# Optimization experiments

Hardware: AMD Instinct MI355X
Metric: run time of the kernel (lower is better)

The kernel has to match this reference:

```python
import jax, jax.numpy as jnp
import numpy as np

NUM_GRAPHS = 512

def setup_inputs() -> dict:
    key = jax.random.key(0)
    ks = jax.random.split(key, 8)
    N, E, SD = 50000, 800000, 128
    x_ids = jax.random.randint(ks[0], (N,), 0, 1340)
    edge_index = jax.random.randint(ks[1], (2, E), 0, N)
    batch = jnp.sort(jax.random.randint(ks[2], (N,), 0, NUM_GRAPHS))
    emb = jax.random.normal(ks[3], (1340, SD), dtype=jnp.float32) * 0.1
    W1 = jax.random.normal(ks[4], (SD, 2 * SD), dtype=jnp.float32) * 0.1
    b1 = jnp.zeros((2 * SD,), dtype=jnp.float32)
    W2 = jax.random.normal(ks[5], (2 * SD, 41), dtype=jnp.float32) * 0.1
    b2 = jnp.zeros((41,), dtype=jnp.float32)
    return {"x_ids": x_ids, "edge_index": edge_index, "batch": batch,
            "emb": emb, "W1": W1, "b1": b1, "W2": W2, "b2": b2}

def _gcn_conv(x, src, dst, W, b, num_nodes):
    # x: [N, Fin] -> [N, Fout]; GCN: add self-loops, deg^-1/2 norm, transform, aggregate
    deg = jax.ops.segment_sum(jnp.ones_like(dst, dtype=x.dtype), dst, num_segments=num_nodes)
    dinv = jnp.where(deg > 0, jax.lax.rsqrt(jnp.where(deg > 0, deg, 1.0)), 0.0)
    norm = dinv[src] * dinv[dst]               # [E+N]
    h = x @ W                                  # [N, Fout]
    msg = h[src] * norm[:, None]               # [E+N, Fout] gather (memory-bound)
    out = jax.ops.segment_sum(msg, dst, num_segments=num_nodes)
    return out + b

def reference(x_ids, edge_index, batch, emb, W1, b1, W2, b2):
    N = x_ids.shape[0]
    loops = jnp.arange(N, dtype=edge_index.dtype)
    src = jnp.concatenate([edge_index[0], loops])
    dst = jnp.concatenate([edge_index[1], loops])
    x = emb[x_ids]                                   # embedding lookup [N, SD]
    x = _gcn_conv(x, src, dst, W1, b1, N)
    x = jax.nn.relu(x)                               # dropout is identity in eval mode
    x = _gcn_conv(x, src, dst, W2, b2, N)
    return jax.ops.segment_sum(x, batch, num_segments=NUM_GRAPHS)  # [512, 41]
```

## Files before the change

kernel.cpp:

```cpp
#include <hip/hip_runtime.h>

#define N_NODES 50000
#define N_EDGES 800000
#define N_TOT   850000
#define SD 128
#define HD 256
#define OD 41
#define ODP 48
#define NG 512
#define NB 128
#define NPB 391
#define BCAP 8192

typedef __attribute__((ext_vector_type(8))) short bh8;
typedef __attribute__((ext_vector_type(4))) float f4;
typedef unsigned long long u64;

__device__ inline unsigned short f2bf(float x) {
  unsigned u = __float_as_uint(x);
  unsigned r = u + 0x7fff + ((u >> 16) & 1);
  return (unsigned short)(r >> 16);
}
__device__ inline float bf2f(unsigned short s) {
  return __uint_as_float(((unsigned)s) << 16);
}
__device__ inline float bflo(unsigned e) { return __uint_as_float(e << 16); }
__device__ inline float bfhi(unsigned e) { return __uint_as_float(e & 0xffff0000u); }

__device__ inline unsigned rec_xid(u64 r)  { return ((unsigned)r) >> 16; }
__device__ inline unsigned rec_src(u64 r)  { return ((unsigned)r) & 0xFFFFu; }
__device__ inline float    rec_nrm(u64 r)  { return __uint_as_float((unsigned)(r >> 32) & 0xFFFF0000u); }

__global__ __launch_bounds__(256) void zero2_kernel(float4* __restrict__ a, int na,
                                                    float4* __restrict__ b, int nb) {
  int i = blockIdx.x * 256 + threadIdx.x;
  float4 z = make_float4(0.f, 0.f, 0.f, 0.f);
  if (i < na) { a[i] = z; return; }
  int j = i - na;
  if (j < nb) b[j] = z;
}

__global__ __launch_bounds__(256) void cvt_all_kernel(const float* __restrict__ emb,
    const float* __restrict__ W1, const float* __restrict__ W2,
    unsigned short* __restrict__ embb, unsigned short* __restrict__ w1f,
    unsigned short* __restrict__ w2f) {
  int tid = blockIdx.x * 256 + threadIdx.x;
  if (tid < 1340 * SD) { embb[tid] = f2bf(emb[tid]); return; }
  int u = tid - 1340 * SD;
  if (u < 4096) {
    int lane = u & 63, frag = u >> 6;
    int ks = frag >> 4, cf = frag & 15;
    int col = cf * 16 + (lane & 15);
    #pragma unroll
    for (int j = 0; j < 8; ++j) {
      int k = ks * 32 + ((lane >> 4) << 3) + j;
      w1f[u * 8 + j] = f2bf(W1[k * HD + col]);
    }
    return;
  }
  u -= 4096;
  if (u < 1536) {
    int lane = u & 63, frag = u >> 6;
    int ks = frag / 3, cf = frag % 3;
    int col = cf * 16 + (lane & 15);
    #pragma unroll
    for (int j = 0; j < 8; ++j) {
      int k = ks * 32 + ((lane >> 4) << 3) + j;
      w2f[u * 8 + j] = (col < OD) ? f2bf(W2[k * OD + col]) : (unsigned short)0;
    }
  }
}

__global__ __launch_bounds__(256) void passA_kernel(const int* __restrict__ ei,
    const int* __restrict__ x_ids, int* __restrict__ curB, u64* __restrict__ stage) {
  __shared__ int lcur[NB];
  __shared__ int base[NB];
  int t = threadIdx.x;
  if (t < NB) lcur[t] = 0;
  __syncthreads();
  u64 pay[16];
  int loc[16];
  int e0 = blockIdx.x * 4096;
  #pragma unroll
  for (int j = 0; j < 16; ++j) {
    int e = e0 + j * 256 + t;
    loc[j] = -1;
    if (e < N_TOT) {
      int s, d;
      if (e < N_EDGES) { s = ei[e]; d = ei[N_EDGES + e]; }
      else             { s = d = e - N_EDGES; }
      int b = d / NPB;
      int lofs = atomicAdd(&lcur[b], 1);
      loc[j] = (b << 13) | lofs;
      pay[j] = ((u64)(unsigned)x_ids[s] << 32) | ((u64)(unsigned)d << 16) | (u64)(unsigned)s;
    }
  }
  __syncthreads();
  if (t < NB) base[t] = atomicAdd(&curB[t], lcur[t]);
  __syncthreads();
  #pragma unroll
  for (int j = 0; j < 16; ++j) {
    if (loc[j] >= 0) {
      int b = loc[j] >> 13, lofs = loc[j] & 8191;
      stage[(size_t)b * BCAP + base[b] + lofs] = pay[j];
    }
  }
}

__global__ __launch_bounds__(256) void count_kernel(const int* __restrict__ curB,
    const u64* __restrict__ stage, int* __restrict__ vcnt, float* __restrict__ dinv) {
  __shared__ int cl[NPB];
  int t = threadIdx.x, k = blockIdx.x;
  for (int l = t; l < NPB; l += 256) cl[l] = 0;
  __syncthreads();
  int nbk = curB[k];
  const u64* st = stage + (size_t)k * BCAP;
  for (int i = t; i < nbk; i += 256) {
    int d = (int)((st[i] >> 16) & 0xFFFFu);
    atomicAdd(&cl[d - k * NPB], 1);
  }
  __syncthreads();
  int n0 = k * NPB;
  int nn = (n0 + NPB <= N_NODES) ? NPB : (N_NODES - n0);
  for (int l = t; l < nn; l += 256) {
    int v = cl[l];
    vcnt[n0 + l] = v;
    dinv[n0 + l] = rsqrtf((float)v);
  }
}

__global__ __launch_bounds__(256) void scan1_kernel(const int* __restrict__ vcnt,
    int* __restrict__ off, int* __restrict__ bsum) {
  __shared__ int lds[256];
  int t = threadIdx.x;
  int i = blockIdx.x * 256 + t;
  int v = (i < N_NODES) ? vcnt[i] : 0;
  lds[t] = v;
  __syncthreads();
  for (int s = 1; s < 256; s <<= 1) {
    int add = (t >= s) ? lds[t - s] : 0;
    __syncthreads();
    lds[t] += add;
    __syncthreads();
  }
  int inc = lds[t];
  if (i < N_NODES) off[i] = inc - v;
  if (t == 255) bsum[blockIdx.x] = inc;
}

__global__ __launch_bounds__(256) void scan2_kernel(int* __restrict__ bsum, int* __restrict__ bso, int nb) {
  __shared__ int lds[256];
  int t = threadIdx.x;
  int v = (t < nb) ? bsum[t] : 0;
  lds[t] = v;
  __syncthreads();
  for (int s = 1; s < 256; s <<= 1) {
    int add = (t >= s) ? lds[t - s] : 0;
    __syncthreads();
    lds[t] += add;
    __syncthreads();
  }
  if (t < nb) bso[t] = lds[t] - v;
}

__global__ __launch_bounds__(256) void scan3g_kernel(int* __restrict__ off,
    const int* __restrict__ bso, const int* __restrict__ batch, int* __restrict__ gstart) {
  int i = blockIdx.x * 256 + threadIdx.x;
  if (i < N_NODES) off[i] += bso[blockIdx.x];
  if (i == 0) off[N_NODES] = N_TOT;
  if (i < N_NODES) {
    if (i == 0) {
      for (int g = 0; g <= batch[0]; ++g) gstart[g] = 0;
    } else {
      int bp = batch[i - 1], bn = batch[i];
      for (int g = bp + 1; g <= bn; ++g) gstart[g] = i;
    }
    if (i == N_NODES - 1) {
      for (int g = batch[i] + 1; g <= NG; ++g) gstart[g] = N_NODES;
    }
  }
}

__global__ __launch_bounds__(256) void passB_kernel(const int* __restrict__ curB,
    const u64* __restrict__ stage, const int* __restrict__ off,
    const float* __restrict__ dinv, u64* __restrict__ rec) {
  __shared__ int lcur[NPB];
  __shared__ int loff[NPB];
  int t = threadIdx.x, k = blockIdx.x;
  int n0 = k * NPB;
  int nn = (n0 + NPB <= N_NODES) ? NPB : (N_NODES - n0);
  for (int l = t; l < nn; l += 256) { lcur[l] = 0; loff[l] = off[n0 + l]; }
  __syncthreads();
  int nbk = curB[k];
  const u64* st = stage + (size_t)k * BCAP;
  for (int i = t; i < nbk; i += 256) {
    u64 r = st[i];
    int s   = (int)(r & 0xFFFFu);
    int d   = (int)((r >> 16) & 0xFFFFu);
    int xid = (int)((r >> 32) & 0xFFFFu);
    float nrm = dinv[s] * dinv[d];
    int ld = d - n0;
    int p = loff[ld] + atomicAdd(&lcur[ld], 1);
    rec[p] = ((u64)f2bf(nrm) << 48) | ((u64)(unsigned)xid << 16) | (u64)(unsigned)s;
  }
}

__global__ __launch_bounds__(256) void agg1w_kernel(const int* __restrict__ off,
    const u64* __restrict__ rec, const unsigned int* __restrict__ embw,
    unsigned int* __restrict__ agg1w) {
  int lane = threadIdx.x & 63;
  int node = __builtin_amdgcn_readfirstlane(blockIdx.x * 4 + (threadIdx.x >> 6));
  int beg = off[node], end = off[node + 1];
  float a0 = 0.f, a1 = 0.f;
  int i = beg;
  for (; i + 8 <= end; i += 8) {
    u64 r[8];
    unsigned e[8];
    #pragma unroll
    for (int p = 0; p < 8; ++p) r[p] = rec[i + p];
    #pragma unroll
    for (int p = 0; p < 8; ++p) e[p] = embw[rec_xid(r[p]) * 64 + lane];
    #pragma unroll
    for (int p = 0; p < 8; ++p) {
      float n = rec_nrm(r[p]);
      a0 += n * bflo(e[p]); a1 += n * bfhi(e[p]);
    }
  }
  for (; i + 4 <= end; i += 4) {
    u64 r0 = rec[i], r1 = rec[i + 1], r2 = rec[i + 2], r3 = rec[i + 3];
    unsigned e0 = embw[rec_xid(r0) * 64 + lane];
    unsigned e1 = embw[rec_xid(r1) * 64 + lane];
    unsigned e2 = embw[rec_xid(r2) * 64 + lane];
    unsigned e3 = embw[rec_xid(r3) * 64 + lane];
    float n0 = rec_nrm(r0), n1 = rec_nrm(r1), n2 = rec_nrm(r2), n3 = rec_nrm(r3);
    a0 += n0 * bflo(e0); a1 += n0 * bfhi(e0);
    a0 += n1 * bflo(e1); a1 += n1 * bfhi(e1);
    a0 += n2 * bflo(e2); a1 += n2 * bfhi(e2);
    a0 += n3 * bflo(e3); a1 += n3 * bfhi(e3);
  }
  for (; i < end; ++i) {
    u64 r = rec[i];
    unsigned e = embw[rec_xid(r) * 64 + lane];
    float n = rec_nrm(r);
    a0 += n * bflo(e); a1 += n * bfhi(e);
  }
  unsigned packed = (unsigned)f2bf(a0) | ((unsigned)f2bf(a1) << 16);
  agg1w[node * 64 + lane] = packed;
}

__global__ __launch_bounds__(256) void gemm12_mfma(const unsigned short* __restrict__ agg1,
    const bh8* __restrict__ w1f, const float* __restrict__ b1,
    const bh8* __restrict__ w2f, unsigned short* __restrict__ h2b) {
  __shared__ char raw[32768];
  int t = threadIdx.x, lane = t & 63, wave = t >> 6;
  int row0 = blockIdx.x * 64;
  #pragma unroll
  for (int k = 0; k < 4; ++k) {
    int idx = k * 256 + t;
    int r = idx >> 4, cc = idx & 15;
    int4 v = make_int4(0, 0, 0, 0);
    if (row0 + r < N_NODES)
      v = *(const int4*)((const char*)agg1 + (size_t)(row0 + r) * 256 + cc * 16);
    *(int4*)(raw + ((r * 256 + cc * 16) ^ ((r & 15) << 4))) = v;
  }
  bh8 bf1[4][4];
  #pragma unroll
  for (int cf = 0; cf < 4; ++cf)
    #pragma unroll
    for (int ks = 0; ks < 4; ++ks)
      bf1[cf][ks] = w1f[(ks * 16 + wave * 4 + cf) * 64 + lane];
  f4 acc[4][4];
  #pragma unroll
  for (int rf = 0; rf < 4; ++rf)
    #pragma unroll
    for (int cf = 0; cf < 4; ++cf)
      acc[rf][cf] = (f4){0.f, 0.f, 0.f, 0.f};
  __syncthreads();
  #pragma unroll
  for (int ks = 0; ks < 4; ++ks) {
    bh8 a[4];
    #pragma unroll
    for (int rf = 0; rf < 4; ++rf) {
      int r = rf * 16 + (lane & 15);
      int byte = (r * 256 + ks * 64 + ((lane >> 4) << 4)) ^ ((r & 15) << 4);
      a[rf] = *(const bh8*)(raw + byte);
    }
    #pragma unroll
    for (int rf = 0; rf < 4; ++rf)
      #pragma unroll
      for (int cf = 0; cf < 4; ++cf)
        acc[rf][cf] = __builtin_amdgcn_mfma_f32_16x16x32_bf16(a[rf], bf1[cf][ks], acc[rf][cf], 0, 0, 0);
  }
  __syncthreads();
  #pragma unroll
  for (int cf = 0; cf < 4; ++cf) {
    int col = wave * 64 + cf * 16 + (lane & 15);
    float bias = b1[col];
    #pragma unroll
    for (int rf = 0; rf < 4; ++rf)
      #pragma unroll
      for (int j = 0; j < 4; ++j) {
        int r = rf * 16 + ((lane >> 4) << 2) + j;
        unsigned short v = f2bf(fmaxf(acc[rf][cf][j] + bias, 0.f));
        *(unsigned short*)(raw + ((r * 512 + col * 2) ^ ((r & 15) << 4))) = v;
      }
  }
  bh8 bf2[3][8];
  #pragma unroll
  for (int cf = 0; cf < 3; ++cf)
    #pragma unroll
    for (int ks = 0; ks < 8; ++ks)
      bf2[cf][ks] = w2f[(ks * 3 + cf) * 64 + lane];
  f4 acc2[3];
  #pragma unroll
  for (int cf = 0; cf < 3; ++cf) acc2[cf] = (f4){0.f, 0.f, 0.f, 0.f};
  __syncthreads();
  int r2 = wave * 16 + (lane & 15);
  #pragma unroll
  for (int ks = 0; ks < 8; ++ks) {
    int byte = (r2 * 512 + ks * 64 + ((lane >> 4) << 4)) ^ ((r2 & 15) << 4);
    bh8 a = *(const bh8*)(raw + byte);
    #pragma unroll
    for (int cf = 0; cf < 3; ++cf)
      acc2[cf] = __builtin_amdgcn_mfma_f32_16x16x32_bf16(a, bf2[cf][ks], acc2[cf], 0, 0, 0);
  }
  #pragma unroll
  for (int cf = 0; cf < 3; ++cf) {
    int col = cf * 16 + (lane & 15);
    #pragma unroll
    for (int j = 0; j < 4; ++j) {
      int rg = row0 + wave * 16 + ((lane >> 4) << 2) + j;
      if (rg < N_NODES)
        h2b[(size_t)rg * ODP + col] = f2bf(acc2[cf][j]);
    }
  }
}

__global__ __launch_bounds__(256) void pool2_kernel(const int* __restrict__ gstart,
    const int* __restrict__ off, const u64* __restrict__ rec,
    const unsigned short* __restrict__ h2b, const float* __restrict__ b2,
    float* __restrict__ out) {
  __shared__ float red[4][2][24][2];
  int g = blockIdx.x >> 3, c = blockIdx.x & 7;
  int t = threadIdx.x, lane = t & 63, wv = t >> 6;
  int n0 = gstart[g], n1 = gstart[g + 1];
  int e0 = off[n0], e1 = off[n1];
  int len = e1 - e0;
  int c0 = e0 + ((len * c) >> 3);
  int c1 = e0 + ((len * (c + 1)) >> 3);
  int clen = c1 - c0;
  int w0 = c0 + ((clen * wv) >> 2);
  int w1 = c0 + ((clen * (wv + 1)) >> 2);
  int half = (lane >= 24 && lane < 48) ? 1 : 0;
  int l24 = (lane < 24) ? lane : ((lane < 48) ? lane - 24 : lane - 48);
  float a0 = 0.f, a1 = 0.f;
  int i = w0;
  for (; i + 16 <= w1; i += 16) {
    u64 ra[8], rb[8];
    #pragma unroll
    for (int p = 0; p < 8; ++p) { ra[p] = rec[i + 2 * p]; rb[p] = rec[i + 2 * p + 1]; }
    #pragma unroll
    for (int p = 0; p < 8; ++p) {
      u64 r = half ? rb[p] : ra[p];
      unsigned hw = *(const unsigned*)(h2b + (size_t)rec_src(r) * ODP + l24 * 2);
      float n = rec_nrm(r);
      a0 += n * bflo(hw); a1 += n * bfhi(hw);
    }
  }
  for (; i < w1; ++i) {
    u64 r = rec[i];
    unsigned hw = *(const unsigned*)(h2b + (size_t)rec_src(r) * ODP + l24 * 2);
    float n = rec_nrm(r);
    if (lane < 24) { a0 += n * bflo(hw); a1 += n * bfhi(hw); }
  }
  if (lane < 48) { red[wv][half][l24][0] = a0; red[wv][half][l24][1] = a1; }
  __syncthreads();
  if (t < 48) {
    int m = t >> 1, b = t & 1;
    float s = red[0][0][m][b] + red[0][1][m][b] + red[1][0][m][b] + red[1][1][m][b]
            + red[2][0][m][b] + red[2][1][m][b] + red[3][0][m][b] + red[3][1][m][b];
    if (t < OD) {
      if (c == 0) s += (float)(n1 - n0) * b2[t];
      unsafeAtomicAdd(&out[g * OD + t], s);
    }
  }
}

extern "C" void kernel_launch(void* const* d_in, const int* in_sizes, int n_in,
                              void* d_out, int out_size, void* d_ws, size_t ws_size,
                              hipStream_t stream) {
  const int*   x_ids = (const int*)d_in[0];
  const int*   ei    = (const int*)d_in[1];
  const int*   batch = (const int*)d_in[2];
  const float* emb   = (const float*)d_in[3];
  const float* W1    = (const float*)d_in[4];
  const float* b1    = (const float*)d_in[5];
  const float* W2    = (const float*)d_in[6];
  const float* b2    = (const float*)d_in[7];
  float* out = (float*)d_out;
  char* ws = (char*)d_ws;

  int*            vcnt   = (int*)           (ws + 0);
  int*            curB   = (int*)           (ws + 204800);
  float*          dinv   = (float*)         (ws + 208896);
  int*            off    = (int*)           (ws + 413696);
  int*            bsum   = (int*)           (ws + 618496);
  int*            bso    = (int*)           (ws + 619520);
  int*            gstart = (int*)           (ws + 620544);
  unsigned short* embb   = (unsigned short*)(ws + 1048576);
  unsigned short* w1f    = (unsigned short*)(ws + 1441792);
  unsigned short* w2f    = (unsigned short*)(ws + 1507328);
  u64*            rec    = (u64*)           (ws + 2097152);
  u64*            stage  = (u64*)           (ws + 9437184);
  unsigned short* agg1   = (unsigned short*)(ws + 18874368);
  unsigned short* h2b    = (unsigned short*)(ws + 33554432);

  zero2_kernel<<<21, 256, 0, stream>>>((float4*)curB, 32, (float4*)out, 5248);
  cvt_all_kernel<<<692, 256, 0, stream>>>(emb, W1, W2, embb, w1f, w2f);

  passA_kernel<<<208, 256, 0, stream>>>(ei, x_ids, curB, stage);
  count_kernel<<<NB,  256, 0, stream>>>(curB, stage, vcnt, dinv);
  scan1_kernel<<<196, 256, 0, stream>>>(vcnt, off, bsum);
  scan2_kernel<<<1,   256, 0, stream>>>(bsum, bso, 196);
  scan3g_kernel<<<196, 256, 0, stream>>>(off, bso, batch, gstart);
  passB_kernel<<<NB,  256, 0, stream>>>(curB, stage, off, dinv, rec);

  agg1w_kernel<<<12500, 256, 0, stream>>>(off, rec, (const unsigned int*)embb, (unsigned int*)agg1);
  gemm12_mfma <<<782,   256, 0, stream>>>(agg1, (const bh8*)w1f, b1, (const bh8*)w2f, h2b);
  pool2_kernel<<<4096,  256, 0, stream>>>(gstart, off, rec, h2b, b2, out);
}
```

Before: 118.2 us.

## Widen gather loads to 16 bytes and fold small setup kernels together

The layer-1 aggregation now has each lane gather a 16-byte chunk of an embedding row, with four edges handled per wave at once, and reduces the partial sums across lanes with shuffles. The pooling pass likewise loads 16-byte chunks of h2 rows, ten edges per wave across 60 lanes, and reduces through a larger shared array. The zeroing kernel is merged into the conversion kernel, and the single-block scan2 is folded into scan3g, where every block redoes the 196-entry scan itself. Together these aim to cut memory instructions and launch count, at the cost of extra shuffle and reduction work and some idle lanes.

```diff
diff --git a/kernel.cpp b/kernel.cpp
--- a/kernel.cpp
+++ b/kernel.cpp
@@ -26,24 +26,18 @@
 }
 __device__ inline float bflo(unsigned e) { return __uint_as_float(e << 16); }
 __device__ inline float bfhi(unsigned e) { return __uint_as_float(e & 0xffff0000u); }
+__device__ inline unsigned pk2(float lo, float hi) {
+  return (unsigned)f2bf(lo) | ((unsigned)f2bf(hi) << 16);
+}
 
 __device__ inline unsigned rec_xid(u64 r)  { return ((unsigned)r) >> 16; }
 __device__ inline unsigned rec_src(u64 r)  { return ((unsigned)r) & 0xFFFFu; }
 __device__ inline float    rec_nrm(u64 r)  { return __uint_as_float((unsigned)(r >> 32) & 0xFFFF0000u); }
 
-__global__ __launch_bounds__(256) void zero2_kernel(float4* __restrict__ a, int na,
-                                                    float4* __restrict__ b, int nb) {
-  int i = blockIdx.x * 256 + threadIdx.x;
-  float4 z = make_float4(0.f, 0.f, 0.f, 0.f);
-  if (i < na) { a[i] = z; return; }
-  int j = i - na;
-  if (j < nb) b[j] = z;
-}
-
-__global__ __launch_bounds__(256) void cvt_all_kernel(const float* __restrict__ emb,
+__global__ __launch_bounds__(256) void init_kernel(const float* __restrict__ emb,
     const float* __restrict__ W1, const float* __restrict__ W2,
     unsigned short* __restrict__ embb, unsigned short* __restrict__ w1f,
-    unsigned short* __restrict__ w2f) {
+    unsigned short* __restrict__ w2f, float4* __restrict__ curB4, float4* __restrict__ out4) {
   int tid = blockIdx.x * 256 + threadIdx.x;
   if (tid < 1340 * SD) { embb[tid] = f2bf(emb[tid]); return; }
   int u = tid - 1340 * SD;
@@ -68,7 +62,13 @@
       int k = ks * 32 + ((lane >> 4) << 3) + j;
       w2f[u * 8 + j] = (col < OD) ? f2bf(W2[k * OD + col]) : (unsigned short)0;
     }
-  }
+    return;
+  }
+  u -= 1536;
+  float4 z = make_float4(0.f, 0.f, 0.f, 0.f);
+  if (u < 32) { curB4[u] = z; return; }
+  u -= 32;
+  if (u < 5248) out4[u] = z;
 }
 
 __global__ __launch_bounds__(256) void passA_kernel(const int* __restrict__ ei,
@@ -148,10 +148,11 @@
   if (t == 255) bsum[blockIdx.x] = inc;
 }
 
-__global__ __launch_bounds__(256) void scan2_kernel(int* __restrict__ bsum, int* __restrict__ bso, int nb) {
+__global__ __launch_bounds__(256) void scan3g_kernel(int* __restrict__ off,
+    const int* __restrict__ bsum, const int* __restrict__ batch, int* __restrict__ gstart) {
   __shared__ int lds[256];
   int t = threadIdx.x;
-  int v = (t < nb) ? bsum[t] : 0;
+  int v = (t < 196) ? bsum[t] : 0;
   lds[t] = v;
   __syncthreads();
   for (int s = 1; s < 256; s <<= 1) {
@@ -160,13 +161,10 @@
     lds[t] += add;
     __syncthreads();
   }
-  if (t < nb) bso[t] = lds[t] - v;
-}
-
-__global__ __launch_bounds__(256) void scan3g_kernel(int* __restrict__ off,
-    const int* __restrict__ bso, const int* __restrict__ batch, int* __restrict__ gstart) {
-  int i = blockIdx.x * 256 + threadIdx.x;
-  if (i < N_NODES) off[i] += bso[blockIdx.x];
+  int b = blockIdx.x;
+  int bso = (b == 0) ? 0 : lds[b - 1];
+  int i = b * 256 + t;
+  if (i < N_NODES) off[i] += bso;
   if (i == 0) off[N_NODES] = N_TOT;
   if (i < N_NODES) {
     if (i == 0) {
@@ -206,46 +204,53 @@
 }
 
 __global__ __launch_bounds__(256) void agg1w_kernel(const int* __restrict__ off,
-    const u64* __restrict__ rec, const unsigned int* __restrict__ embw,
-    unsigned int* __restrict__ agg1w) {
+    const u64* __restrict__ rec, const uint4* __restrict__ emb16,
+    uint4* __restrict__ agg16) {
   int lane = threadIdx.x & 63;
   int node = __builtin_amdgcn_readfirstlane(blockIdx.x * 4 + (threadIdx.x >> 6));
   int beg = off[node], end = off[node + 1];
-  float a0 = 0.f, a1 = 0.f;
+  int eslot = lane >> 4, fgrp = lane & 15;
+  float a[8];
+  #pragma unroll
+  for (int j = 0; j < 8; ++j) a[j] = 0.f;
   int i = beg;
   for (; i + 8 <= end; i += 8) {
-    u64 r[8];
-    unsigned e[8];
-    #pragma unroll
-    for (int p = 0; p < 8; ++p) r[p] = rec[i + p];
-    #pragma unroll
-    for (int p = 0; p < 8; ++p) e[p] = embw[rec_xid(r[p]) * 64 + lane];
-    #pragma unroll
-    for (int p = 0; p < 8; ++p) {
-      float n = rec_nrm(r[p]);
-      a0 += n * bflo(e[p]); a1 += n * bfhi(e[p]);
-    }
-  }
-  for (; i + 4 <= end; i += 4) {
-    u64 r0 = rec[i], r1 = rec[i + 1], r2 = rec[i + 2], r3 = rec[i + 3];
-    unsigned e0 = embw[rec_xid(r0) * 64 + lane];
-    unsigned e1 = embw[rec_xid(r1) * 64 + lane];
-    unsigned e2 = embw[rec_xid(r2) * 64 + lane];
-    unsigned e3 = embw[rec_xid(r3) * 64 + lane];
-    float n0 = rec_nrm(r0), n1 = rec_nrm(r1), n2 = rec_nrm(r2), n3 = rec_nrm(r3);
-    a0 += n0 * bflo(e0); a1 += n0 * bfhi(e0);
-    a0 += n1 * bflo(e1); a1 += n1 * bfhi(e1);
-    a0 += n2 * bflo(e2); a1 += n2 * bfhi(e2);
-    a0 += n3 * bflo(e3); a1 += n3 * bfhi(e3);
-  }
-  for (; i < end; ++i) {
-    u64 r = rec[i];
-    unsigned e = embw[rec_xid(r) * 64 + lane];
-    float n = rec_nrm(r);
-    a0 += n * bflo(e); a1 += n * bfhi(e);
-  }
-  unsigned packed = (unsigned)f2bf(a0) | ((unsigned)f2bf(a1) << 16);
-  agg1w[node * 64 + lane] = packed;
+    u64 rA = rec[i + eslot];
+    u64 rB = rec[i + 4 + eslot];
+    uint4 vA = emb16[rec_xid(rA) * 16 + fgrp];
+    uint4 vB = emb16[rec_xid(rB) * 16 + fgrp];
+    float nA = rec_nrm(rA), nB = rec_nrm(rB);
+    a[0] += nA * bflo(vA.x); a[1] += nA * bfhi(vA.x);
+    a[2] += nA * bflo(vA.y); a[3] += nA * bfhi(vA.y);
+    a[4] += nA * bflo(vA.z); a[5] += nA * bfhi(vA.z);
+    a[6] += nA * bflo(vA.w); a[7] += nA * bfhi(vA.w);
+    a[0] += nB * bflo(vB.x); a[1] += nB * bfhi(vB.x);
+    a[2] += nB * bflo(vB.y); a[3] += nB * bfhi(vB.y);
+    a[4] += nB * bflo(vB.z); a[5] += nB * bfhi(vB.z);
+    a[6] += nB * bflo(vB.w); a[7] += nB * bfhi(vB.w);
+  }
+  for (; i < end; i += 4) {
+    int idx = i + eslot;
+    bool val = idx < end;
+    u64 r = rec[val ? idx : (end - 1)];
+    uint4 v = emb16[rec_xid(r) * 16 + fgrp];
+    float n = val ? rec_nrm(r) : 0.f;
+    a[0] += n * bflo(v.x); a[1] += n * bfhi(v.x);
+    a[2] += n * bflo(v.y); a[3] += n * bfhi(v.y);
+    a[4] += n * bflo(v.z); a[5] += n * bfhi(v.z);
+    a[6] += n * bflo(v.w); a[7] += n * bfhi(v.w);
+  }
+  #pragma unroll
+  for (int j = 0; j < 8; ++j) {
+    a[j] += __shfl_xor(a[j], 16);
+    a[j] += __shfl_xor(a[j], 32);
+  }
+  if (lane < 16) {
+    uint4 o;
+    o.x = pk2(a[0], a[1]); o.y = pk2(a[2], a[3]);
+    o.z = pk2(a[4], a[5]); o.w = pk2(a[6], a[7]);
+    agg16[(size_t)node * 16 + fgrp] = o;
+  }
 }
 
 __global__ __launch_bounds__(256) void gemm12_mfma(const unsigned short* __restrict__ agg1,
@@ -340,7 +345,7 @@
     const int* __restrict__ off, const u64* __restrict__ rec,
     const unsigned short* __restrict__ h2b, const float* __restrict__ b2,
     float* __restrict__ out) {
-  __shared__ float red[4][2][24][2];
+  __shared__ float red[4][60][8];
   int g = blockIdx.x >> 3, c = blockIdx.x & 7;
   int t = threadIdx.x, lane = t & 63, wv = t >> 6;
   int n0 = gstart[g], n1 = gstart[g + 1];
@@ -351,34 +356,46 @@
   int clen = c1 - c0;
   int w0 = c0 + ((clen * wv) >> 2);
   int w1 = c0 + ((clen * (wv + 1)) >> 2);
-  int half = (lane >= 24 && lane < 48) ? 1 : 0;
-  int l24 = (lane < 24) ? lane : ((lane < 48) ? lane - 24 : lane - 48);
-  float a0 = 0.f, a1 = 0.f;
+  bool live = lane < 60;
+  int eslot = live ? lane / 6 : 0;
+  int fgrp  = live ? lane - (lane / 6) * 6 : 0;
+  float a[8];
+  #pragma unroll
+  for (int j = 0; j < 8; ++j) a[j] = 0.f;
   int i = w0;
-  for (; i + 16 <= w1; i += 16) {
-    u64 ra[8], rb[8];
-    #pragma unroll
-    for (int p = 0; p < 8; ++p) { ra[p] = rec[i + 2 * p]; rb[p] = rec[i + 2 * p + 1]; }
-    #pragma unroll
-    for (int p = 0; p < 8; ++p) {
-      u64 r = half ? rb[p] : ra[p];
-      unsigned hw = *(const unsigned*)(h2b + (size_t)rec_src(r) * ODP + l24 * 2);
-      float n = rec_nrm(r);
-      a0 += n * bflo(hw); a1 += n * bfhi(hw);
-    }
-  }
-  for (; i < w1; ++i) {
-    u64 r = rec[i];
-    unsigned hw = *(const unsigned*)(h2b + (size_t)rec_src(r) * ODP + l24 * 2);
-    float n = rec_nrm(r);
-    if (lane < 24) { a0 += n * bflo(hw); a1 += n * bfhi(hw); }
-  }
-  if (lane < 48) { red[wv][half][l24][0] = a0; red[wv][half][l24][1] = a1; }
+  for (; i + 10 <= w1; i += 10) {
+    u64 r = rec[i + eslot];
+    uint4 v = *(const uint4*)(h2b + (size_t)rec_src(r) * ODP + fgrp * 8);
+    float n = live ? rec_nrm(r) : 0.f;
+    a[0] += n * bflo(v.x); a[1] += n * bfhi(v.x);
+    a[2] += n * bflo(v.y); a[3] += n * bfhi(v.y);
+    a[4] += n * bflo(v.z); a[5] += n * bfhi(v.z);
+    a[6] += n * bflo(v.w); a[7] += n * bfhi(v.w);
+  }
+  if (i < w1) {
+    int idx = i + eslot;
+    bool val = live && idx < w1;
+    u64 r = rec[val ? idx : w0];
+    uint4 v = *(const uint4*)(h2b + (size_t)rec_src(r) * ODP + fgrp * 8);
+    float n = val ? rec_nrm(r) : 0.f;
+    a[0] += n * bflo(v.x); a[1] += n * bfhi(v.x);
+    a[2] += n * bflo(v.y); a[3] += n * bfhi(v.y);
+    a[4] += n * bflo(v.z); a[5] += n * bfhi(v.z);
+    a[6] += n * bflo(v.w); a[7] += n * bfhi(v.w);
+  }
+  if (live) {
+    #pragma unroll
+    for (int j = 0; j < 8; ++j) red[wv][lane][j] = a[j];
+  }
   __syncthreads();
   if (t < 48) {
-    int m = t >> 1, b = t & 1;
-    float s = red[0][0][m][b] + red[0][1][m][b] + red[1][0][m][b] + red[1][1][m][b]
-            + red[2][0][m][b] + red[2][1][m][b] + red[3][0][m][b] + red[3][1][m][b];
+    int fg = t >> 3, j = t & 7;
+    float s = 0.f;
+    #pragma unroll
+    for (int w = 0; w < 4; ++w)
+      #pragma unroll
+      for (int e = 0; e < 10; ++e)
+        s += red[w][e * 6 + fg][j];
     if (t < OD) {
       if (c == 0) s += (float)(n1 - n0) * b2[t];
       unsafeAtomicAdd(&out[g * OD + t], s);
@@ -405,7 +422,6 @@
   float*          dinv   = (float*)         (ws + 208896);
   int*            off    = (int*)           (ws + 413696);
   int*            bsum   = (int*)           (ws + 618496);
-  int*            bso    = (int*)           (ws + 619520);
   int*            gstart = (int*)           (ws + 620544);
   unsigned short* embb   = (unsigned short*)(ws + 1048576);
   unsigned short* w1f    = (unsigned short*)(ws + 1441792);
@@ -415,17 +431,15 @@
   unsigned short* agg1   = (unsigned short*)(ws + 18874368);
   unsigned short* h2b    = (unsigned short*)(ws + 33554432);
 
-  zero2_kernel<<<21, 256, 0, stream>>>((float4*)curB, 32, (float4*)out, 5248);
-  cvt_all_kernel<<<692, 256, 0, stream>>>(emb, W1, W2, embb, w1f, w2f);
-
+  init_kernel <<<713, 256, 0, stream>>>(emb, W1, W2, embb, w1f, w2f,
+                                        (float4*)curB, (float4*)out);
   passA_kernel<<<208, 256, 0, stream>>>(ei, x_ids, curB, stage);
   count_kernel<<<NB,  256, 0, stream>>>(curB, stage, vcnt, dinv);
   scan1_kernel<<<196, 256, 0, stream>>>(vcnt, off, bsum);
-  scan2_kernel<<<1,   256, 0, stream>>>(bsum, bso, 196);
-  scan3g_kernel<<<196, 256, 0, stream>>>(off, bso, batch, gstart);
+  scan3g_kernel<<<196, 256, 0, stream>>>(off, bsum, batch, gstart);
   passB_kernel<<<NB,  256, 0, stream>>>(curB, stage, off, dinv, rec);
 
-  agg1w_kernel<<<12500, 256, 0, stream>>>(off, rec, (const unsigned int*)embb, (unsigned int*)agg1);
+  agg1w_kernel<<<12500, 256, 0, stream>>>(off, rec, (const uint4*)embb, (uint4*)agg1);
   gemm12_mfma <<<782,   256, 0, stream>>>(agg1, (const bh8*)w1f, b1, (const bh8*)w2f, h2b);
   pool2_kernel<<<4096,  256, 0, stream>>>(gstart, off, rec, h2b, b2, out);
 }
```

Measured after the change: 106.0 us. -10.4%, faster.
